# Kernel tuning notes

Measured on AMD Instinct MI355X. Metric: run time of the kernel, lower is better.

## Reference

```python
import jax, jax.numpy as jnp
import numpy as np

BUCKETS = 64
DIM = 512  # self.dim, used only for attention scaling


def setup_inputs() -> dict:
    key = jax.random.key(0)
    k1, k2, k3, k4 = jax.random.split(key, 4)
    b, h, t, dh = 4, 8, 8192, 64
    q = jax.random.normal(k1, (b, h, t, dh), dtype=jnp.float32)
    k = jax.random.normal(k2, (b, h, t, dh), dtype=jnp.float32)
    v = jax.random.normal(k3, (b, h, t, dh), dtype=jnp.float32)
    W = jax.random.normal(k4, (1, h, 2 * dh, BUCKETS), dtype=jnp.float32)  # SimpleSortNet.linear
    return {"q": q, "k": k, "v": v, "W": W}


def reference(q, k, v, W):
    b, h, t, dh = q.shape
    bh = b * h
    bsz = t // BUCKETS  # bucket size = 128

    # merge batch and heads, then bucket: [bh, buckets, bsz, dh]
    b_q = q.reshape(bh, BUCKETS, bsz, dh)
    b_k = k.reshape(bh, BUCKETS, bsz, dh)
    b_v = v.reshape(bh, BUCKETS, bsz, dh)

    # --- SimpleSortNet (non_permutative=True -> softmax, no gumbel) ---
    # summarize each bucket by sum over tokens, concat q/k summaries
    x = jnp.concatenate([b_q.sum(axis=2), b_k.sum(axis=2)], axis=-1)  # [bh, buckets, 2*dh]
    Wb = jnp.broadcast_to(W, (b, h, 2 * dh, BUCKETS)).reshape(bh, 2 * dh, BUCKETS)
    R = jax.nn.relu(jnp.einsum('bud,bdv->buv', x, Wb))  # [bh, buckets, buckets]
    R = jax.nn.softmax(R, axis=-1)

    # zero_all_but_top: keep only top-1 entry along last dim (dim=2)
    top_idx = jnp.argmax(R, axis=-1)  # [bh, buckets]
    top_mask = jnp.arange(BUCKETS) == top_idx[..., None]
    R = jnp.where(top_mask, R, jnp.zeros((), dtype=R.dtype))

    # reorder key/value buckets by (sparsified) R
    b_k_r = jnp.einsum('buv,bvtd->butd', R, b_k)
    b_v_r = jnp.einsum('buv,bvtd->butd', R, b_v)

    # buckets == kv_buckets: attend over [reordered bucket ; own bucket]
    bk = jnp.concatenate([b_k_r, b_k], axis=2)  # [bh, buckets, 2*bsz, dh]
    bv = jnp.concatenate([b_v_r, b_v], axis=2)

    # bucketed attention; note: original scales by self.dim ** -0.5 (full dim)
    dots = jnp.einsum('buie,buje->buij', b_q, bk) * (DIM ** -0.5)
    attn = jax.nn.softmax(dots, axis=-1)
    out = jnp.einsum('buij,buje->buie', attn, bv)  # [bh, buckets, bsz, dh]

    return out.reshape(b, h, t, dh)
```

## Files before the change

kernel.cpp:

```cpp
#include <hip/hip_runtime.h>


#define T_TOK 8192
#define CQ (0.04419417382415922f * 1.4426950408889634f)
#define FIXED_M 12.0f

#define KB_OFF 0
#define VT_OFF 16384
#define XB_OFF 32768
#define QP_OFF 33280
#define KP_OFF 34304

typedef __attribute__((ext_vector_type(16))) float f32x16;
typedef __attribute__((ext_vector_type(8))) short bf16x8;

__device__ __forceinline__ unsigned cvtpk(float lo, float hi) {
  unsigned r;
  asm("v_cvt_pk_bf16_f32 %0, %1, %2" : "=v"(r) : "v"(lo), "v"(hi));
  return r;
}
__device__ __forceinline__ float exp2v(float x) {
  float r;
  asm("v_exp_f32 %0, %1\n\ts_nop 0" : "=v"(r) : "v"(x));
  return r;
}

#define ATTN_TILE(TLOC, VUHALF)                                                \
  {                                                                            \
    int tokr = (TLOC) * 32 + ln;                                               \
    f32x16 acc;                                                                \
    _Pragma("unroll") for (int r = 0; r < 16; ++r) acc[r] = 0.f;               \
    __builtin_amdgcn_s_setprio(1);                                             \
    _Pragma("unroll") for (int sl = 0; sl < 4; ++sl) {                         \
      int addr =                                                               \
          KB_OFF + tokr * 128 + ((sl * 32 + lhi * 16) ^ ((tokr & 7) << 4));    \
      bf16x8 af = *reinterpret_cast<const bf16x8*>(smem + addr);               \
      acc = __builtin_amdgcn_mfma_f32_32x32x16_bf16(af, qf[sl], acc, 0, 0, 0); \
    }                                                                          \
    _Pragma("unroll") for (int r = 0; r < 16; ++r) {                           \
      float lg = (VUHALF) ? acc[r] * ru : acc[r];                              \
      float p = exp2v(lg - FIXED_M);                                           \
      acc[r] = p;                                                              \
      lsum += p;                                                               \
    }                                                                          \
    _Pragma("unroll") for (int ks = 0; ks < 2; ++ks) {                         \
      int r0 = 8 * ks;                                                         \
      unsigned aA, bA, aB, bB;                                                 \
      asm("v_cvt_pk_bf16_f32 %0, %1, %2"                                       \
          : "=v"(aA) : "v"(acc[r0 + 0]), "v"(acc[r0 + 1]));                    \
      asm("v_cvt_pk_bf16_f32 %0, %1, %2"                                       \
          : "=v"(bA) : "v"(acc[r0 + 2]), "v"(acc[r0 + 3]));                    \
      asm("v_cvt_pk_bf16_f32 %0, %1, %2"                                       \
          : "=v"(aB) : "v"(acc[r0 + 4]), "v"(acc[r0 + 5]));                    \
      asm("v_cvt_pk_bf16_f32 %0, %1, %2"                                       \
          : "=v"(bB) : "v"(acc[r0 + 6]), "v"(acc[r0 + 7]));                    \
      asm("s_nop 1\n\tv_permlane32_swap_b32 %0, %1\n\ts_nop 1"                 \
          : "+v"(aA), "+v"(aB));                                               \
      asm("s_nop 1\n\tv_permlane32_swap_b32 %0, %1\n\ts_nop 1"                 \
          : "+v"(bA), "+v"(bB));                                               \
      union { unsigned uu[4]; bf16x8 f; } pf;                                  \
      pf.uu[0] = aA; pf.uu[1] = bA; pf.uu[2] = aB; pf.uu[3] = bB;              \
      int t2 = 2 * ((TLOC) * 32 + ks * 16 + lhi * 8);                          \
      {                                                                        \
        int d = ln;                                                            \
        int addr = VT_OFF + d * 256 + (t2 ^ ((d & 15) << 4));                  \
        bf16x8 vf = *reinterpret_cast<const bf16x8*>(smem + addr);             \
        o0 = __builtin_amdgcn_mfma_f32_32x32x16_bf16(pf.f, vf, o0, 0, 0, 0);   \
      }                                                                        \
      {                                                                        \
        int d = 32 + ln;                                                       \
        int addr = VT_OFF + d * 256 + (t2 ^ ((d & 15) << 4));                  \
        bf16x8 vf = *reinterpret_cast<const bf16x8*>(smem + addr);             \
        o1 = __builtin_amdgcn_mfma_f32_32x32x16_bf16(pf.f, vf, o1, 0, 0, 0);   \
      }                                                                        \
    }                                                                          \
    __builtin_amdgcn_s_setprio(0);                                             \
  }

__global__ __launch_bounds__(256, 2) void k3_attn(
    const float* __restrict__ q, const float* __restrict__ k,
    const float* __restrict__ v, const float* __restrict__ W,
    float* __restrict__ out) {
  __shared__ unsigned char smem[38400];

  int L = blockIdx.x;
  int G = ((L & 7) << 8) | (L >> 3);
  int bhi = G >> 6, u = G & 63;
  int tid = threadIdx.x;
  int l = tid & 63;
  int w = tid >> 6;
  int lhi = l >> 5;
  int ln = l & 31;
  int hh = bhi & 7;

  const float* kb = k + (size_t)bhi * (T_TOK * 64);
  const float* vb = v + (size_t)bhi * (T_TOK * 64);
  int c4 = tid & 15;
  int tp = tid >> 2;

  const float* qrow = q + ((size_t)bhi * T_TOK + (size_t)u * 128 + w * 32 + ln) * 64;
  float4 qld[8];
  #pragma unroll
  for (int sl = 0; sl < 4; ++sl) {
    qld[2 * sl] = *reinterpret_cast<const float4*>(qrow + sl * 16 + lhi * 8);
    qld[2 * sl + 1] = *reinterpret_cast<const float4*>(qrow + sl * 16 + lhi * 8 + 4);
  }
  float4 kld[8];
  #pragma unroll
  for (int it = 0; it < 8; ++it) {
    int row = (tid >> 4) + it * 16;
    kld[it] = *reinterpret_cast<const float4*>(
        kb + (size_t)(u * 128 + row) * 64 + c4 * 4);
  }
  float4 vld[8];
  {
    const float* s0 = vb + ((size_t)(u * 128 + 2 * tp)) * 64 + (tid & 3) * 4;
    #pragma unroll
    for (int i = 0; i < 4; ++i) {
      vld[i] = *reinterpret_cast<const float4*>(s0 + i * 16);
      vld[4 + i] = *reinterpret_cast<const float4*>(s0 + i * 16 + 64);
    }
  }

  bf16x8 qf[4];
  float qs[32];
  #pragma unroll
  for (int sl = 0; sl < 4; ++sl) {
    float4 a4 = qld[2 * sl], b4 = qld[2 * sl + 1];
    qs[sl * 8 + 0] = a4.x; qs[sl * 8 + 1] = a4.y;
    qs[sl * 8 + 2] = a4.z; qs[sl * 8 + 3] = a4.w;
    qs[sl * 8 + 4] = b4.x; qs[sl * 8 + 5] = b4.y;
    qs[sl * 8 + 6] = b4.z; qs[sl * 8 + 7] = b4.w;
    union { unsigned uu[4]; bf16x8 f; } qu;
    qu.uu[0] = cvtpk(a4.x * CQ, a4.y * CQ);
    qu.uu[1] = cvtpk(a4.z * CQ, a4.w * CQ);
    qu.uu[2] = cvtpk(b4.x * CQ, b4.y * CQ);
    qu.uu[3] = cvtpk(b4.z * CQ, b4.w * CQ);
    qf[sl] = qu.f;
  }
  #pragma unroll
  for (int off = 1; off < 32; off <<= 1) {
    #pragma unroll
    for (int j = 0; j < 32; ++j) qs[j] += __shfl_xor(qs[j], off, 64);
  }
  if (ln == 0) {
    float* qp = (float*)(smem + QP_OFF) + w * 64 + lhi * 8;
    #pragma unroll
    for (int sl = 0; sl < 4; ++sl) {
      #pragma unroll
      for (int j = 0; j < 8; ++j) qp[sl * 16 + j] = qs[sl * 8 + j];
    }
  }

  float4 ksum = make_float4(0.f, 0.f, 0.f, 0.f);
  #pragma unroll
  for (int it = 0; it < 8; ++it) {
    float4 val = kld[it];
    ksum.x += val.x; ksum.y += val.y; ksum.z += val.z; ksum.w += val.w;
    int row = (tid >> 4) + it * 16;
    int addr = KB_OFF + row * 128 + ((c4 * 8) ^ ((row & 7) << 4));
    *reinterpret_cast<uint2*>(smem + addr) =
        make_uint2(cvtpk(val.x, val.y), cvtpk(val.z, val.w));
  }
  *reinterpret_cast<float4*>(smem + KP_OFF + tid * 16) = ksum;

  #pragma unroll
  for (int i = 0; i < 4; ++i) {
    int dq = (tid & 3) + 4 * i;
    int t2 = 4 * tp;
    const float* fa = (const float*)&vld[i];
    const float* fc = (const float*)&vld[4 + i];
    #pragma unroll
    for (int jj = 0; jj < 4; ++jj) {
      int d = dq * 4 + jj;
      int addr = VT_OFF + d * 256 + (t2 ^ ((d & 15) << 4));
      *reinterpret_cast<unsigned*>(smem + addr) = cvtpk(fa[jj], fc[jj]);
    }
  }

  __syncthreads();

  if (tid < 128) {
    float* xbw = (float*)(smem + XB_OFF);
    if (tid < 64) {
      const float* qp = (const float*)(smem + QP_OFF);
      xbw[tid] = qp[tid] + qp[64 + tid] + qp[128 + tid] + qp[192 + tid];
    } else {
      int d = tid - 64;
      const float* kp = (const float*)(smem + KP_OFF);
      float xk = 0.f;
      #pragma unroll
      for (int g = 0; g < 16; ++g) xk += kp[(g * 16 + (d >> 2)) * 4 + (d & 3)];
      xbw[64 + d] = xk;
    }
  }
  __syncthreads();

  const float* xb = (const float*)(smem + XB_OFF);
  const float* wcol = W + (size_t)hh * 8192 + l;
  float a0 = 0.f, a1 = 0.f, a2 = 0.f, a3 = 0.f;
  #pragma unroll
  for (int kk = 0; kk < 128; kk += 4) {
    a0 = fmaf(xb[kk + 0], wcol[(size_t)(kk + 0) * 64], a0);
    a1 = fmaf(xb[kk + 1], wcol[(size_t)(kk + 1) * 64], a1);
    a2 = fmaf(xb[kk + 2], wcol[(size_t)(kk + 2) * 64], a2);
    a3 = fmaf(xb[kk + 3], wcol[(size_t)(kk + 3) * 64], a3);
  }
  float a = fmaxf((a0 + a1) + (a2 + a3), 0.f);
  float bvv = a; int bi = l;
  #pragma unroll
  for (int off = 1; off < 64; off <<= 1) {
    float ov = __shfl_xor(bvv, off, 64);
    int oi = __shfl_xor(bi, off, 64);
    if (ov > bvv || (ov == bvv && oi < bi)) { bvv = ov; bi = oi; }
  }
  float e = __expf(a - bvv);
  #pragma unroll
  for (int off = 1; off < 64; off <<= 1) e += __shfl_xor(e, off, 64);
  int vu = bi;
  float ru = 1.f / e;

  float4 kvu[8];
  #pragma unroll
  for (int it = 0; it < 8; ++it) {
    int row = (tid >> 4) + it * 16;
    kvu[it] = *reinterpret_cast<const float4*>(
        kb + (size_t)(vu * 128 + row) * 64 + c4 * 4);
  }
  float4 vvu[8];
  {
    const float* s0 = vb + ((size_t)(vu * 128 + 2 * tp)) * 64 + (tid & 3) * 4;
    #pragma unroll
    for (int i = 0; i < 4; ++i) {
      vvu[i] = *reinterpret_cast<const float4*>(s0 + i * 16);
      vvu[4 + i] = *reinterpret_cast<const float4*>(s0 + i * 16 + 64);
    }
  }

  f32x16 o0, o1;
  #pragma unroll
  for (int r = 0; r < 16; ++r) { o0[r] = 0.f; o1[r] = 0.f; }
  float lsum = 0.f;

  #pragma unroll
  for (int t8 = 0; t8 < 4; ++t8) ATTN_TILE(t8, false)

  __syncthreads();

  #pragma unroll
  for (int it = 0; it < 8; ++it) {
    int row = (tid >> 4) + it * 16;
    int addr = KB_OFF + row * 128 + ((c4 * 8) ^ ((row & 7) << 4));
    *reinterpret_cast<uint2*>(smem + addr) =
        make_uint2(cvtpk(kvu[it].x, kvu[it].y), cvtpk(kvu[it].z, kvu[it].w));
  }
  #pragma unroll
  for (int i = 0; i < 4; ++i) {
    int dq = (tid & 3) + 4 * i;
    int t2 = 4 * tp;
    const float* fa = (const float*)&vvu[i];
    const float* fc = (const float*)&vvu[4 + i];
    #pragma unroll
    for (int jj = 0; jj < 4; ++jj) {
      int d = dq * 4 + jj;
      int addr = VT_OFF + d * 256 + (t2 ^ ((d & 15) << 4));
      *reinterpret_cast<unsigned*>(smem + addr) = cvtpk(fa[jj] * ru, fc[jj] * ru);
    }
  }
  __syncthreads();

  #pragma unroll
  for (int t8 = 0; t8 < 4; ++t8) ATTN_TILE(t8, true)

  lsum += __shfl_xor(lsum, 32, 64);
  float inv = 1.f / lsum;
  float* ob = out + ((size_t)bhi * T_TOK + (size_t)u * 128 + w * 32) * 64;
  #pragma unroll
  for (int r = 0; r < 16; ++r) {
    int row = (r & 3) + 8 * (r >> 2) + 4 * lhi;
    float invr = __shfl(inv, row, 64);
    ob[(size_t)row * 64 + ln] = o0[r] * invr;
    ob[(size_t)row * 64 + 32 + ln] = o1[r] * invr;
  }
}

extern "C" void kernel_launch(void* const* d_in, const int* in_sizes, int n_in,
                              void* d_out, int out_size, void* d_ws, size_t ws_size,
                              hipStream_t stream) {
  const float* q = (const float*)d_in[0];
  const float* k = (const float*)d_in[1];
  const float* v = (const float*)d_in[2];
  const float* W = (const float*)d_in[3];
  float* out = (float*)d_out;

  hipLaunchKernelGGL(k3_attn, dim3(2048), dim3(256), 0, stream, q, k, v, W, out);
}
```

Baseline: 66.82 us.

## Double-buffer K/V shared tiles and stagger block start with s_sleep

Splits the shared-memory K and V^T staging into two buffers, so the reordered bucket's K/V can be written while other waves are still reading the own-bucket tiles. This removes one __syncthreads between the two attention phases. It also adds a staggered s_sleep at block start, keyed on block index, to spread out memory request bursts. Shared memory grows from about 38 KB to about 71 KB per block, which may stop two blocks from fitting on one CU and adds idle cycles at launch.

```diff
diff --git a/kernel.cpp b/kernel.cpp
--- a/kernel.cpp
+++ b/kernel.cpp
@@ -5,11 +5,13 @@
 #define CQ (0.04419417382415922f * 1.4426950408889634f)
 #define FIXED_M 12.0f
 
-#define KB_OFF 0
-#define VT_OFF 16384
-#define XB_OFF 32768
-#define QP_OFF 33280
-#define KP_OFF 34304
+#define KB0_OFF 0
+#define VT0_OFF 16384
+#define KB1_OFF 32768
+#define VT1_OFF 49152
+#define XB_OFF 65536
+#define QP_OFF 66048
+#define KP_OFF 67072
 
 typedef __attribute__((ext_vector_type(16))) float f32x16;
 typedef __attribute__((ext_vector_type(8))) short bf16x8;
@@ -25,7 +27,7 @@
   return r;
 }
 
-#define ATTN_TILE(TLOC, VUHALF)                                                \
+#define ATTN_TILE(TLOC, VUHALF, KBO, VTO)                                      \
   {                                                                            \
     int tokr = (TLOC) * 32 + ln;                                               \
     f32x16 acc;                                                                \
@@ -33,7 +35,7 @@
     __builtin_amdgcn_s_setprio(1);                                             \
     _Pragma("unroll") for (int sl = 0; sl < 4; ++sl) {                         \
       int addr =                                                               \
-          KB_OFF + tokr * 128 + ((sl * 32 + lhi * 16) ^ ((tokr & 7) << 4));    \
+          (KBO) + tokr * 128 + ((sl * 32 + lhi * 16) ^ ((tokr & 7) << 4));     \
       bf16x8 af = *reinterpret_cast<const bf16x8*>(smem + addr);               \
       acc = __builtin_amdgcn_mfma_f32_32x32x16_bf16(af, qf[sl], acc, 0, 0, 0); \
     }                                                                          \
@@ -63,13 +65,13 @@
       int t2 = 2 * ((TLOC) * 32 + ks * 16 + lhi * 8);                          \
       {                                                                        \
         int d = ln;                                                            \
-        int addr = VT_OFF + d * 256 + (t2 ^ ((d & 15) << 4));                  \
+        int addr = (VTO) + d * 256 + (t2 ^ ((d & 15) << 4));                   \
         bf16x8 vf = *reinterpret_cast<const bf16x8*>(smem + addr);             \
         o0 = __builtin_amdgcn_mfma_f32_32x32x16_bf16(pf.f, vf, o0, 0, 0, 0);   \
       }                                                                        \
       {                                                                        \
         int d = 32 + ln;                                                       \
-        int addr = VT_OFF + d * 256 + (t2 ^ ((d & 15) << 4));                  \
+        int addr = (VTO) + d * 256 + (t2 ^ ((d & 15) << 4));                   \
         bf16x8 vf = *reinterpret_cast<const bf16x8*>(smem + addr);             \
         o1 = __builtin_amdgcn_mfma_f32_32x32x16_bf16(pf.f, vf, o1, 0, 0, 0);   \
       }                                                                        \
@@ -81,9 +83,15 @@
     const float* __restrict__ q, const float* __restrict__ k,
     const float* __restrict__ v, const float* __restrict__ W,
     float* __restrict__ out) {
-  __shared__ unsigned char smem[38400];
+  __shared__ unsigned char smem[71168];
 
   int L = blockIdx.x;
+  {
+    int g = ((L >> 3) ^ (L >> 8)) & 3;
+    if (g == 1) __builtin_amdgcn_s_sleep(16);
+    else if (g == 2) __builtin_amdgcn_s_sleep(32);
+    else if (g == 3) __builtin_amdgcn_s_sleep(48);
+  }
   int G = ((L & 7) << 8) | (L >> 3);
   int bhi = G >> 6, u = G & 63;
   int tid = threadIdx.x;
@@ -158,7 +166,7 @@
     float4 val = kld[it];
     ksum.x += val.x; ksum.y += val.y; ksum.z += val.z; ksum.w += val.w;
     int row = (tid >> 4) + it * 16;
-    int addr = KB_OFF + row * 128 + ((c4 * 8) ^ ((row & 7) << 4));
+    int addr = KB0_OFF + row * 128 + ((c4 * 8) ^ ((row & 7) << 4));
     *reinterpret_cast<uint2*>(smem + addr) =
         make_uint2(cvtpk(val.x, val.y), cvtpk(val.z, val.w));
   }
@@ -173,7 +181,7 @@
     #pragma unroll
     for (int jj = 0; jj < 4; ++jj) {
       int d = dq * 4 + jj;
-      int addr = VT_OFF + d * 256 + (t2 ^ ((d & 15) << 4));
+      int addr = VT0_OFF + d * 256 + (t2 ^ ((d & 15) << 4));
       *reinterpret_cast<unsigned*>(smem + addr) = cvtpk(fa[jj], fc[jj]);
     }
   }
@@ -243,14 +251,12 @@
   float lsum = 0.f;
 
   #pragma unroll
-  for (int t8 = 0; t8 < 4; ++t8) ATTN_TILE(t8, false)
-
-  __syncthreads();
+  for (int t8 = 0; t8 < 4; ++t8) ATTN_TILE(t8, false, KB0_OFF, VT0_OFF)
 
   #pragma unroll
   for (int it = 0; it < 8; ++it) {
     int row = (tid >> 4) + it * 16;
-    int addr = KB_OFF + row * 128 + ((c4 * 8) ^ ((row & 7) << 4));
+    int addr = KB1_OFF + row * 128 + ((c4 * 8) ^ ((row & 7) << 4));
     *reinterpret_cast<uint2*>(smem + addr) =
         make_uint2(cvtpk(kvu[it].x, kvu[it].y), cvtpk(kvu[it].z, kvu[it].w));
   }
@@ -263,14 +269,14 @@
     #pragma unroll
     for (int jj = 0; jj < 4; ++jj) {
       int d = dq * 4 + jj;
-      int addr = VT_OFF + d * 256 + (t2 ^ ((d & 15) << 4));
+      int addr = VT1_OFF + d * 256 + (t2 ^ ((d & 15) << 4));
       *reinterpret_cast<unsigned*>(smem + addr) = cvtpk(fa[jj] * ru, fc[jj] * ru);
     }
   }
   __syncthreads();
 
   #pragma unroll
-  for (int t8 = 0; t8 < 4; ++t8) ATTN_TILE(t8, true)
+  for (int t8 = 0; t8 < 4; ++t8) ATTN_TILE(t8, true, KB1_OFF, VT1_OFF)
 
   lsum += __shfl_xor(lsum, 32, 64);
   float inv = 1.f / lsum;
```

Result: slower. 71.01 us (+6.3%).
